# Performance work log

Measured on AMD Instinct MI355X. Metric: run time of the kernel, lower is better.

The kernel has to match this reference:

```python
import jax, jax.numpy as jnp
import numpy as np

G = 16        # groups / heads
DG = 128      # per-group dim (2048/16)
F = 2048      # feat dim (representation_size)
N = 2048      # num_rois
M = 2048      # num_nongt_rois


def setup_inputs() -> dict:
    key = jax.random.key(0)
    ks = jax.random.split(key, 8)
    std = np.float32(0.02)
    return {
        "roi_feat": jax.random.normal(ks[0], (N, F), jnp.float32),
        "ref_feat": jax.random.normal(ks[1], (M, F), jnp.float32),
        "Wq_w": jax.random.normal(ks[2], (F, F), jnp.float32) * std,
        "Wq_b": jnp.zeros((F,), jnp.float32),
        "Wk_w": jax.random.normal(ks[3], (F, F), jnp.float32) * std,
        "Wk_b": jnp.zeros((F,), jnp.float32),
        # grouped 1x1 conv weight [2048, 2048, 1, 1] squeezed to [F, F];
        # group g maps input channels [g*F_g_in] -> output channels [g*DG:(g+1)*DG]
        "Wv_w": jax.random.normal(ks[4], (F, F), jnp.float32) * np.float32(0.01),
        "Wv_b": jnp.zeros((F,), jnp.float32),
    }


def reference(roi_feat, ref_feat, Wq_w, Wq_b, Wk_w, Wk_b, Wv_w, Wv_b):
    n = roi_feat.shape[0]
    scale = np.float32(1.0 / np.sqrt(DG))
    # torch Linear: y = x @ W.T + b
    q = (roi_feat @ Wq_w.T + Wq_b).reshape(n, G, DG)      # [N, G, DG]
    k = (ref_feat @ Wk_w.T + Wk_b).reshape(-1, G, DG)     # [M, G, DG]
    aff = jnp.einsum("ngd,mgd->ngm", q, k) * scale        # [N, G, M]
    attn = jax.nn.softmax(aff, axis=-1)
    # weighted values: v is raw ref_feat, per original
    ov = jnp.einsum("ngm,mf->ngf", attn, ref_feat)        # [N, G, F]
    # grouped 1x1 conv: per-group linear F -> DG
    Wv3 = Wv_w.reshape(G, DG, F)                          # [G, DG, F]
    out = jnp.einsum("ngf,gdf->ngd", ov, Wv3) + Wv_b.reshape(G, DG)
    return out.reshape(n, G * DG)                          # [N, F]
```

## Files before the change

### kernel.cpp

```cpp
#include <hip/hip_runtime.h>
#include <hip/hip_bf16.h>

#define G_   16
#define DG_  128
#define F_   2048
#define N_   2048
#define M_   2048

typedef __attribute__((ext_vector_type(8))) short s16x8;
typedef __attribute__((ext_vector_type(4))) float f32x4;
typedef __attribute__((ext_vector_type(2))) unsigned int u32x2;

typedef const __attribute__((address_space(1))) void GV;
typedef __attribute__((address_space(3))) void LV;

__device__ inline unsigned short f2bf(float f) {
  unsigned u = __float_as_uint(f);
  u += 0x7fffu + ((u >> 16) & 1u);
  return (unsigned short)(u >> 16);
}

struct Cvt5Args { const float* s[5]; unsigned short* d[5]; };

__global__ __launch_bounds__(256)
void cvt5(Cvt5Args a) {
  unsigned u = blockIdx.x * 256 + threadIdx.x;
  if (u >= 5u * 524288u) return;
  int seg = u >> 19;
  unsigned off = u & 524287u;
  const float4* sp = (const float4*)(a.s[seg] + (size_t)off * 8);
  float4 x = sp[0], y = sp[1];
  uint4 o;
  o.x = (unsigned)f2bf(x.x) | ((unsigned)f2bf(x.y) << 16);
  o.y = (unsigned)f2bf(x.z) | ((unsigned)f2bf(x.w) << 16);
  o.z = (unsigned)f2bf(y.x) | ((unsigned)f2bf(y.y) << 16);
  o.w = (unsigned)f2bf(y.z) | ((unsigned)f2bf(y.w) << 16);
  *(uint4*)(a.d[seg] + (size_t)off * 8) = o;
}

struct GemmJobs {
  const unsigned short* A[3];
  const unsigned short* B[3];
  const float* bias[3];
  unsigned short* C[3];
  float osc[3];
};

__global__ __launch_bounds__(512, 2)
void gemm8(GemmJobs jb) {
  __shared__ __align__(16) char lds[131072];
  const int wg = (blockIdx.x & 7) * 24 + (blockIdx.x >> 3);
  const int j  = wg >> 6;
  const int bs = wg & 63;
  const unsigned short* A = jb.A[j];
  const unsigned short* B = jb.B[j];
  const float* bias = jb.bias[j];
  unsigned short* C = jb.C[j];
  const float osc = jb.osc[j];

  const int tid = threadIdx.x, lane = tid & 63, wv = tid >> 6;
  const int wm = wv >> 2, wn = wv & 3;
  const int l15 = lane & 15, l4 = lane >> 4;
  const int m0 = (bs >> 3) * 256, n0 = (bs & 7) * 256;
  const int slot = (l4 ^ ((l15 >> 1) & 3)) * 16;
  const int scol = (((lane & 3) ^ ((lane >> 3) & 3)) * 8);
  const int srow = wv * 16 + (lane >> 2);
  const int rA = wm * 128 + l15;
  const int rB = (wn >> 1) * 128 + (wn & 1) * 64 + l15;

  f32x4 acc[8][4];
#pragma unroll
  for (int i = 0; i < 8; ++i)
#pragma unroll
    for (int nf = 0; nf < 4; ++nf) acc[i][nf] = (f32x4){0.f, 0.f, 0.f, 0.f};

  auto stage_kh = [&](int buf2, int h, int k0) {
#pragma unroll
    for (int rb = 0; rb < 2; ++rb) {
      __builtin_amdgcn_global_load_lds(
          (GV*)(A + (size_t)(m0 + rb * 128 + srow) * F_ + k0 + h * 32 + scol),
          (LV*)(lds + buf2 * 65536 + h * 16384 + rb * 8192 + wv * 1024),
          16, 0, 0);
      __builtin_amdgcn_global_load_lds(
          (GV*)(B + (size_t)(n0 + rb * 128 + srow) * F_ + k0 + h * 32 + scol),
          (LV*)(lds + buf2 * 65536 + 32768 + h * 16384 + rb * 8192 + wv * 1024),
          16, 0, 0);
    }
  };

  stage_kh(0, 0, 0);
  stage_kh(0, 1, 0);
  asm volatile("s_waitcnt vmcnt(4)" ::: "memory");
  __builtin_amdgcn_sched_barrier(0);
  __builtin_amdgcn_s_barrier();

  const int NT = F_ / 64;
  for (int t = 0; t < NT; ++t) {
    const int buf = t & 1;
    const char* Lb = lds + buf * 65536;
    const bool pf = (t + 1 < NT);
    const int k1 = (t + 1) * 64;
    s16x8 af[8], bf[4];

    auto ldA = [&](int mf, int h) {
      return *(const s16x8*)(Lb + h * 16384 + (rA + mf * 16) * 64 + slot);
    };
    auto ldB = [&](int nf, int h) {
      return *(const s16x8*)(Lb + 32768 + h * 16384 + (rB + nf * 16) * 64 + slot);
    };

#pragma unroll
    for (int nf = 0; nf < 4; ++nf) bf[nf] = ldB(nf, 0);
#pragma unroll
    for (int i = 0; i < 8; ++i) af[i] = ldA(i, 0);
    if (pf) stage_kh(buf ^ 1, 0, k1);
    __builtin_amdgcn_sched_barrier(0);
    __builtin_amdgcn_s_barrier();
    asm volatile("s_waitcnt lgkmcnt(0)" ::: "memory");
    __builtin_amdgcn_sched_barrier(0);
    __builtin_amdgcn_s_setprio(1);
#pragma unroll
    for (int i = 0; i < 8; ++i)
#pragma unroll
      for (int nf = 0; nf < 4; ++nf)
        acc[i][nf] = __builtin_amdgcn_mfma_f32_16x16x32_bf16(af[i], bf[nf], acc[i][nf], 0, 0, 0);
    __builtin_amdgcn_s_setprio(0);
    __builtin_amdgcn_sched_barrier(0);

    if (pf) { asm volatile("s_waitcnt vmcnt(4)" ::: "memory"); }
    else    { asm volatile("s_waitcnt vmcnt(0)" ::: "memory"); }
    __builtin_amdgcn_sched_barrier(0);
    __builtin_amdgcn_s_barrier();
#pragma unroll
    for (int nf = 0; nf < 4; ++nf) bf[nf] = ldB(nf, 1);
#pragma unroll
    for (int i = 0; i < 8; ++i) af[i] = ldA(i, 1);
    if (pf) stage_kh(buf ^ 1, 1, k1);
    __builtin_amdgcn_sched_barrier(0);
    __builtin_amdgcn_s_barrier();
    asm volatile("s_waitcnt lgkmcnt(0)" ::: "memory");
    __builtin_amdgcn_sched_barrier(0);
    __builtin_amdgcn_s_setprio(1);
#pragma unroll
    for (int i = 0; i < 8; ++i)
#pragma unroll
      for (int nf = 0; nf < 4; ++nf)
        acc[i][nf] = __builtin_amdgcn_mfma_f32_16x16x32_bf16(af[i], bf[nf], acc[i][nf], 0, 0, 0);
    __builtin_amdgcn_s_setprio(0);
    __builtin_amdgcn_sched_barrier(0);

    if (pf) { asm volatile("s_waitcnt vmcnt(4)" ::: "memory"); }
    __builtin_amdgcn_sched_barrier(0);
    __builtin_amdgcn_s_barrier();
  }

#pragma unroll
  for (int nf = 0; nf < 4; ++nf) {
    int c = n0 + wn * 64 + nf * 16 + l15;
    float bv = bias ? bias[c] : 0.f;
#pragma unroll
    for (int mf = 0; mf < 8; ++mf) {
#pragma unroll
      for (int jj = 0; jj < 4; ++jj) {
        int r = m0 + wm * 128 + mf * 16 + l4 * 4 + jj;
        C[(size_t)r * F_ + c] = f2bf((acc[mf][nf][jj] + bv) * osc);
      }
    }
  }
}

__global__ __launch_bounds__(256, 2)
void attn_mfma(const unsigned short* __restrict__ Q,
               const unsigned short* __restrict__ K,
               const unsigned short* __restrict__ Vt,
               const float* __restrict__ vb,
               float* __restrict__ out) {
  __shared__ unsigned short Kt[2][64 * 128];
  __shared__ unsigned short Vts[2][128 * 64];
  __shared__ unsigned short Pt[4][16 * 64];
  const int tid = threadIdx.x, lane = tid & 63, wv = tid >> 6;
  const int l15 = lane & 15, l4 = lane >> 4;
  const int g = blockIdx.y;
  const int q0 = blockIdx.x * 64 + wv * 16;

  s16x8 qa[4];
#pragma unroll
  for (int kc = 0; kc < 4; ++kc)
    qa[kc] = *(const s16x8*)(Q + (size_t)(q0 + l15) * F_ + g * DG_ + kc * 32 + l4 * 8);

  f32x4 oa[8];
#pragma unroll
  for (int df = 0; df < 8; ++df) oa[df] = (f32x4){0.f, 0.f, 0.f, 0.f};
  float m_r = -1e30f, l_r = 0.f;

  const int ksw0 = (((lane & 15) ^ (lane >> 4)) * 8);
  const int ksw1 = (((lane & 15) ^ 4 ^ (lane >> 4)) * 8);
  const int vsw  = (((lane & 7) ^ (lane >> 3)) * 8);
  const int xorb = (l15 & 7) << 4;
  int csw[4];
#pragma unroll
  for (int kc = 0; kc < 4; ++kc) csw[kc] = (kc * 64 + l4 * 16) ^ xorb;

  auto stage = [&](int buf, int kv0) {
#pragma unroll
    for (int i = 0; i < 4; ++i) {
      int r0 = wv * 16 + i * 4;
      __builtin_amdgcn_global_load_lds(
          (GV*)(K + (size_t)(kv0 + r0 + (lane >> 4)) * F_ + g * DG_ + ((i & 1) ? ksw1 : ksw0)),
          (LV*)(&Kt[buf][r0 * 128]), 16, 0, 0);
    }
#pragma unroll
    for (int i = 0; i < 4; ++i) {
      int r0 = wv * 32 + i * 8;
      __builtin_amdgcn_global_load_lds(
          (GV*)(Vt + (size_t)(g * DG_ + r0 + (lane >> 3)) * M_ + kv0 + vsw),
          (LV*)(&Vts[buf][r0 * 64]), 16, 0, 0);
    }
  };

  stage(0, 0);
  __syncthreads();
  int cur = 0;
  unsigned short* Pw = &Pt[wv][0];

  for (int t = 0; t < M_ / 64; ++t) {
    if (t + 1 < M_ / 64) stage(cur ^ 1, (t + 1) * 64);
    const unsigned short* Kb = &Kt[cur][0];
    const unsigned short* Vb = &Vts[cur][0];

    f32x4 sf[4];
    __builtin_amdgcn_s_setprio(1);
#pragma unroll
    for (int kvf = 0; kvf < 4; ++kvf) {
      f32x4 s = (f32x4){0.f, 0.f, 0.f, 0.f};
#pragma unroll
      for (int kc = 0; kc < 4; ++kc) {
        s16x8 kf = *(const s16x8*)((const char*)Kb + (kvf * 16 + l15) * 256 + csw[kc]);
        s = __builtin_amdgcn_mfma_f32_16x16x32_bf16(kf, qa[kc], s, 0, 0, 0);
      }
      sf[kvf] = s;
    }
    __builtin_amdgcn_s_setprio(0);

    float tmax = sf[0][0];
#pragma unroll
    for (int kvf = 0; kvf < 4; ++kvf) {
      tmax = fmaxf(tmax, fmaxf(fmaxf(sf[kvf][0], sf[kvf][1]),
                               fmaxf(sf[kvf][2], sf[kvf][3])));
    }
    tmax = fmaxf(tmax, __shfl_xor(tmax, 16));
    tmax = fmaxf(tmax, __shfl_xor(tmax, 32));
    if (!__all(tmax <= m_r + 8.0f)) {
      float mnew = fmaxf(m_r, tmax);
      float corr = __builtin_amdgcn_exp2f(m_r - mnew);
      m_r = mnew;
      l_r *= corr;
      float c0 = __shfl(corr, l4 * 4 + 0);
      float c1 = __shfl(corr, l4 * 4 + 1);
      float c2 = __shfl(corr, l4 * 4 + 2);
      float c3 = __shfl(corr, l4 * 4 + 3);
#pragma unroll
      for (int df = 0; df < 8; ++df) {
        oa[df][0] *= c0; oa[df][1] *= c1; oa[df][2] *= c2; oa[df][3] *= c3;
      }
    }

    float psum = 0.f;
#pragma unroll
    for (int kvf = 0; kvf < 4; ++kvf) {
      float p0 = __builtin_amdgcn_exp2f(sf[kvf][0] - m_r);
      float p1 = __builtin_amdgcn_exp2f(sf[kvf][1] - m_r);
      float p2 = __builtin_amdgcn_exp2f(sf[kvf][2] - m_r);
      float p3 = __builtin_amdgcn_exp2f(sf[kvf][3] - m_r);
      psum += (p0 + p1) + (p2 + p3);
      u32x2 w;
      asm("v_cvt_pk_bf16_f32 %0, %1, %2" : "=v"(w.x) : "v"(p0), "v"(p1));
      asm("v_cvt_pk_bf16_f32 %0, %1, %2" : "=v"(w.y) : "v"(p2), "v"(p3));
      *(u32x2*)((char*)Pw + l15 * 128 + ((kvf * 32 + l4 * 8) ^ xorb)) = w;
    }
    psum += __shfl_xor(psum, 16);
    psum += __shfl_xor(psum, 32);
    l_r += psum;

    s16x8 pa0 = *(const s16x8*)((const char*)Pw + l15 * 128 + csw[0]);
    s16x8 pa1 = *(const s16x8*)((const char*)Pw + l15 * 128 + csw[1]);
    __builtin_amdgcn_s_setprio(1);
#pragma unroll
    for (int df = 0; df < 8; ++df) {
      s16x8 v0 = *(const s16x8*)((const char*)Vb + (df * 16 + l15) * 128 + csw[0]);
      s16x8 v1 = *(const s16x8*)((const char*)Vb + (df * 16 + l15) * 128 + csw[1]);
      oa[df] = __builtin_amdgcn_mfma_f32_16x16x32_bf16(pa0, v0, oa[df], 0, 0, 0);
      oa[df] = __builtin_amdgcn_mfma_f32_16x16x32_bf16(pa1, v1, oa[df], 0, 0, 0);
    }
    __builtin_amdgcn_s_setprio(0);
    __syncthreads();
    cur ^= 1;
  }

  float linv = 1.0f / l_r;
  float i0 = __shfl(linv, l4 * 4 + 0);
  float i1 = __shfl(linv, l4 * 4 + 1);
  float i2 = __shfl(linv, l4 * 4 + 2);
  float i3 = __shfl(linv, l4 * 4 + 3);
#pragma unroll
  for (int df = 0; df < 8; ++df) {
    int c = g * DG_ + df * 16 + l15;
    float bv = vb[c];
    out[(size_t)(q0 + l4 * 4 + 0) * F_ + c] = oa[df][0] * i0 + bv;
    out[(size_t)(q0 + l4 * 4 + 1) * F_ + c] = oa[df][1] * i1 + bv;
    out[(size_t)(q0 + l4 * 4 + 2) * F_ + c] = oa[df][2] * i2 + bv;
    out[(size_t)(q0 + l4 * 4 + 3) * F_ + c] = oa[df][3] * i3 + bv;
  }
}

extern "C" void kernel_launch(void* const* d_in, const int* in_sizes, int n_in,
                              void* d_out, int out_size, void* d_ws, size_t ws_size,
                              hipStream_t stream) {
  const float* roi  = (const float*)d_in[0];
  const float* ref  = (const float*)d_in[1];
  const float* Wq_w = (const float*)d_in[2];
  const float* Wq_b = (const float*)d_in[3];
  const float* Wk_w = (const float*)d_in[4];
  const float* Wk_b = (const float*)d_in[5];
  const float* Wv_w = (const float*)d_in[6];
  const float* Wv_b = (const float*)d_in[7];
  float* out = (float*)d_out;
  const size_t SEG = 4194304;
  const float cscale = 0.12751664508246770f;

  if (ws_size < 64ull * 1024 * 1024) return;
  unsigned short* roi_bf = (unsigned short*)d_ws;
  unsigned short* ref_bf = roi_bf + SEG;
  unsigned short* Wq_bf  = ref_bf + SEG;
  unsigned short* Wk_bf  = Wq_bf + SEG;
  unsigned short* Wv_bf  = Wk_bf + SEG;
  unsigned short* Qb     = Wv_bf + SEG;
  unsigned short* Kb     = Qb + SEG;
  unsigned short* Vtb    = Kb + SEG;

  Cvt5Args ca;
  ca.s[0] = roi;  ca.d[0] = roi_bf;
  ca.s[1] = ref;  ca.d[1] = ref_bf;
  ca.s[2] = Wq_w; ca.d[2] = Wq_bf;
  ca.s[3] = Wk_w; ca.d[3] = Wk_bf;
  ca.s[4] = Wv_w; ca.d[4] = Wv_bf;
  cvt5<<<10240, 256, 0, stream>>>(ca);

  GemmJobs jb;
  jb.A[0] = roi_bf; jb.B[0] = Wq_bf;  jb.bias[0] = Wq_b;    jb.C[0] = Qb;  jb.osc[0] = cscale;
  jb.A[1] = ref_bf; jb.B[1] = Wk_bf;  jb.bias[1] = Wk_b;    jb.C[1] = Kb;  jb.osc[1] = 1.0f;
  jb.A[2] = Wv_bf;  jb.B[2] = ref_bf; jb.bias[2] = nullptr; jb.C[2] = Vtb; jb.osc[2] = 1.0f;
  gemm8<<<192, 512, 0, stream>>>(jb);

  attn_mfma<<<dim3(N_ / 64, G_), 256, 0, stream>>>(Qb, Kb, Vtb, Wv_b, out);
}
```

Before: 143.1 us.

## Process two 16-row query fragments per wave to reuse K/V LDS reads

Each wave now handles 32 query rows (two 16-row MFMA fragments) instead of 16, so every K and V fragment loaded from LDS feeds two MFMAs. The block covers 128 queries and the grid halves to 256 blocks. This cuts LDS read traffic and staging per unit of work, but raises register pressure (double accumulators and score tiles) and halves the block count, which may lower occupancy on a 256-CU device.

New measurement: 149.9 us. 4.7% more time.

```diff
diff --git a/kernel.cpp b/kernel.cpp
--- a/kernel.cpp
+++ b/kernel.cpp
@@ -177,21 +177,25 @@
                float* __restrict__ out) {
   __shared__ unsigned short Kt[2][64 * 128];
   __shared__ unsigned short Vts[2][128 * 64];
-  __shared__ unsigned short Pt[4][16 * 64];
+  __shared__ unsigned short Pt[4][32 * 64];
   const int tid = threadIdx.x, lane = tid & 63, wv = tid >> 6;
   const int l15 = lane & 15, l4 = lane >> 4;
   const int g = blockIdx.y;
-  const int q0 = blockIdx.x * 64 + wv * 16;
-
-  s16x8 qa[4];
-#pragma unroll
-  for (int kc = 0; kc < 4; ++kc)
-    qa[kc] = *(const s16x8*)(Q + (size_t)(q0 + l15) * F_ + g * DG_ + kc * 32 + l4 * 8);
-
-  f32x4 oa[8];
-#pragma unroll
-  for (int df = 0; df < 8; ++df) oa[df] = (f32x4){0.f, 0.f, 0.f, 0.f};
-  float m_r = -1e30f, l_r = 0.f;
+  const int q0 = blockIdx.x * 128 + wv * 32;
+
+  s16x8 qa[2][4];
+#pragma unroll
+  for (int qf = 0; qf < 2; ++qf)
+#pragma unroll
+    for (int kc = 0; kc < 4; ++kc)
+      qa[qf][kc] = *(const s16x8*)(Q + (size_t)(q0 + qf * 16 + l15) * F_ + g * DG_ + kc * 32 + l4 * 8);
+
+  f32x4 oa[8][2];
+#pragma unroll
+  for (int df = 0; df < 8; ++df)
+#pragma unroll
+    for (int qf = 0; qf < 2; ++qf) oa[df][qf] = (f32x4){0.f, 0.f, 0.f, 0.f};
+  float m_r[2] = {-1e30f, -1e30f}, l_r[2] = {0.f, 0.f};
 
   const int ksw0 = (((lane & 15) ^ (lane >> 4)) * 8);
   const int ksw1 = (((lane & 15) ^ 4 ^ (lane >> 4)) * 8);
@@ -228,88 +232,115 @@
     const unsigned short* Kb = &Kt[cur][0];
     const unsigned short* Vb = &Vts[cur][0];
 
-    f32x4 sf[4];
+    f32x4 sf[4][2];
     __builtin_amdgcn_s_setprio(1);
 #pragma unroll
     for (int kvf = 0; kvf < 4; ++kvf) {
-      f32x4 s = (f32x4){0.f, 0.f, 0.f, 0.f};
+      s16x8 kf[4];
+#pragma unroll
+      for (int kc = 0; kc < 4; ++kc)
+        kf[kc] = *(const s16x8*)((const char*)Kb + (kvf * 16 + l15) * 256 + csw[kc]);
+      f32x4 s0 = (f32x4){0.f, 0.f, 0.f, 0.f};
+      f32x4 s1 = (f32x4){0.f, 0.f, 0.f, 0.f};
 #pragma unroll
       for (int kc = 0; kc < 4; ++kc) {
-        s16x8 kf = *(const s16x8*)((const char*)Kb + (kvf * 16 + l15) * 256 + csw[kc]);
-        s = __builtin_amdgcn_mfma_f32_16x16x32_bf16(kf, qa[kc], s, 0, 0, 0);
+        s0 = __builtin_amdgcn_mfma_f32_16x16x32_bf16(kf[kc], qa[0][kc], s0, 0, 0, 0);
+        s1 = __builtin_amdgcn_mfma_f32_16x16x32_bf16(kf[kc], qa[1][kc], s1, 0, 0, 0);
       }
-      sf[kvf] = s;
+      sf[kvf][0] = s0;
+      sf[kvf][1] = s1;
     }
     __builtin_amdgcn_s_setprio(0);
 
-    float tmax = sf[0][0];
-#pragma unroll
-    for (int kvf = 0; kvf < 4; ++kvf) {
-      tmax = fmaxf(tmax, fmaxf(fmaxf(sf[kvf][0], sf[kvf][1]),
-                               fmaxf(sf[kvf][2], sf[kvf][3])));
-    }
-    tmax = fmaxf(tmax, __shfl_xor(tmax, 16));
-    tmax = fmaxf(tmax, __shfl_xor(tmax, 32));
-    if (!__all(tmax <= m_r + 8.0f)) {
-      float mnew = fmaxf(m_r, tmax);
-      float corr = __builtin_amdgcn_exp2f(m_r - mnew);
-      m_r = mnew;
-      l_r *= corr;
-      float c0 = __shfl(corr, l4 * 4 + 0);
-      float c1 = __shfl(corr, l4 * 4 + 1);
-      float c2 = __shfl(corr, l4 * 4 + 2);
-      float c3 = __shfl(corr, l4 * 4 + 3);
-#pragma unroll
-      for (int df = 0; df < 8; ++df) {
-        oa[df][0] *= c0; oa[df][1] *= c1; oa[df][2] *= c2; oa[df][3] *= c3;
+    float tmax[2];
+#pragma unroll
+    for (int qf = 0; qf < 2; ++qf) {
+      float tm = sf[0][qf][0];
+#pragma unroll
+      for (int kvf = 0; kvf < 4; ++kvf)
+        tm = fmaxf(tm, fmaxf(fmaxf(sf[kvf][qf][0], sf[kvf][qf][1]),
+                             fmaxf(sf[kvf][qf][2], sf[kvf][qf][3])));
+      tm = fmaxf(tm, __shfl_xor(tm, 16));
+      tm = fmaxf(tm, __shfl_xor(tm, 32));
+      tmax[qf] = tm;
+    }
+    if (!__all(tmax[0] <= m_r[0] + 8.0f && tmax[1] <= m_r[1] + 8.0f)) {
+#pragma unroll
+      for (int qf = 0; qf < 2; ++qf) {
+        float mnew = fmaxf(m_r[qf], tmax[qf]);
+        float corr = __builtin_amdgcn_exp2f(m_r[qf] - mnew);
+        m_r[qf] = mnew;
+        l_r[qf] *= corr;
+        float c0 = __shfl(corr, l4 * 4 + 0);
+        float c1 = __shfl(corr, l4 * 4 + 1);
+        float c2 = __shfl(corr, l4 * 4 + 2);
+        float c3 = __shfl(corr, l4 * 4 + 3);
+#pragma unroll
+        for (int df = 0; df < 8; ++df) {
+          oa[df][qf][0] *= c0; oa[df][qf][1] *= c1;
+          oa[df][qf][2] *= c2; oa[df][qf][3] *= c3;
+        }
       }
     }
 
-    float psum = 0.f;
-#pragma unroll
-    for (int kvf = 0; kvf < 4; ++kvf) {
-      float p0 = __builtin_amdgcn_exp2f(sf[kvf][0] - m_r);
-      float p1 = __builtin_amdgcn_exp2f(sf[kvf][1] - m_r);
-      float p2 = __builtin_amdgcn_exp2f(sf[kvf][2] - m_r);
-      float p3 = __builtin_amdgcn_exp2f(sf[kvf][3] - m_r);
-      psum += (p0 + p1) + (p2 + p3);
-      u32x2 w;
-      asm("v_cvt_pk_bf16_f32 %0, %1, %2" : "=v"(w.x) : "v"(p0), "v"(p1));
-      asm("v_cvt_pk_bf16_f32 %0, %1, %2" : "=v"(w.y) : "v"(p2), "v"(p3));
-      *(u32x2*)((char*)Pw + l15 * 128 + ((kvf * 32 + l4 * 8) ^ xorb)) = w;
-    }
-    psum += __shfl_xor(psum, 16);
-    psum += __shfl_xor(psum, 32);
-    l_r += psum;
-
-    s16x8 pa0 = *(const s16x8*)((const char*)Pw + l15 * 128 + csw[0]);
-    s16x8 pa1 = *(const s16x8*)((const char*)Pw + l15 * 128 + csw[1]);
+#pragma unroll
+    for (int qf = 0; qf < 2; ++qf) {
+      float psum = 0.f;
+#pragma unroll
+      for (int kvf = 0; kvf < 4; ++kvf) {
+        float p0 = __builtin_amdgcn_exp2f(sf[kvf][qf][0] - m_r[qf]);
+        float p1 = __builtin_amdgcn_exp2f(sf[kvf][qf][1] - m_r[qf]);
+        float p2 = __builtin_amdgcn_exp2f(sf[kvf][qf][2] - m_r[qf]);
+        float p3 = __builtin_amdgcn_exp2f(sf[kvf][qf][3] - m_r[qf]);
+        psum += (p0 + p1) + (p2 + p3);
+        u32x2 w;
+        asm("v_cvt_pk_bf16_f32 %0, %1, %2" : "=v"(w.x) : "v"(p0), "v"(p1));
+        asm("v_cvt_pk_bf16_f32 %0, %1, %2" : "=v"(w.y) : "v"(p2), "v"(p3));
+        *(u32x2*)((char*)Pw + (qf * 16 + l15) * 128 + ((kvf * 32 + l4 * 8) ^ xorb)) = w;
+      }
+      psum += __shfl_xor(psum, 16);
+      psum += __shfl_xor(psum, 32);
+      l_r[qf] += psum;
+    }
+
+    s16x8 pa[2][2];
+#pragma unroll
+    for (int qf = 0; qf < 2; ++qf)
+#pragma unroll
+      for (int kc2 = 0; kc2 < 2; ++kc2)
+        pa[qf][kc2] = *(const s16x8*)((const char*)Pw + (qf * 16 + l15) * 128 + csw[kc2]);
     __builtin_amdgcn_s_setprio(1);
 #pragma unroll
     for (int df = 0; df < 8; ++df) {
       s16x8 v0 = *(const s16x8*)((const char*)Vb + (df * 16 + l15) * 128 + csw[0]);
       s16x8 v1 = *(const s16x8*)((const char*)Vb + (df * 16 + l15) * 128 + csw[1]);
-      oa[df] = __builtin_amdgcn_mfma_f32_16x16x32_bf16(pa0, v0, oa[df], 0, 0, 0);
-      oa[df] = __builtin_amdgcn_mfma_f32_16x16x32_bf16(pa1, v1, oa[df], 0, 0, 0);
+      oa[df][0] = __builtin_amdgcn_mfma_f32_16x16x32_bf16(pa[0][0], v0, oa[df][0], 0, 0, 0);
+      oa[df][0] = __builtin_amdgcn_mfma_f32_16x16x32_bf16(pa[0][1], v1, oa[df][0], 0, 0, 0);
+      oa[df][1] = __builtin_amdgcn_mfma_f32_16x16x32_bf16(pa[1][0], v0, oa[df][1], 0, 0, 0);
+      oa[df][1] = __builtin_amdgcn_mfma_f32_16x16x32_bf16(pa[1][1], v1, oa[df][1], 0, 0, 0);
     }
     __builtin_amdgcn_s_setprio(0);
     __syncthreads();
     cur ^= 1;
   }
 
-  float linv = 1.0f / l_r;
-  float i0 = __shfl(linv, l4 * 4 + 0);
-  float i1 = __shfl(linv, l4 * 4 + 1);
-  float i2 = __shfl(linv, l4 * 4 + 2);
-  float i3 = __shfl(linv, l4 * 4 + 3);
-#pragma unroll
-  for (int df = 0; df < 8; ++df) {
-    int c = g * DG_ + df * 16 + l15;
-    float bv = vb[c];
-    out[(size_t)(q0 + l4 * 4 + 0) * F_ + c] = oa[df][0] * i0 + bv;
-    out[(size_t)(q0 + l4 * 4 + 1) * F_ + c] = oa[df][1] * i1 + bv;
-    out[(size_t)(q0 + l4 * 4 + 2) * F_ + c] = oa[df][2] * i2 + bv;
-    out[(size_t)(q0 + l4 * 4 + 3) * F_ + c] = oa[df][3] * i3 + bv;
+#pragma unroll
+  for (int qf = 0; qf < 2; ++qf) {
+    float linv = 1.0f / l_r[qf];
+    float i0 = __shfl(linv, l4 * 4 + 0);
+    float i1 = __shfl(linv, l4 * 4 + 1);
+    float i2 = __shfl(linv, l4 * 4 + 2);
+    float i3 = __shfl(linv, l4 * 4 + 3);
+#pragma unroll
+    for (int df = 0; df < 8; ++df) {
+      int c = g * DG_ + df * 16 + l15;
+      float bv = vb[c];
+      int r = q0 + qf * 16 + l4 * 4;
+      out[(size_t)(r + 0) * F_ + c] = oa[df][qf][0] * i0 + bv;
+      out[(size_t)(r + 1) * F_ + c] = oa[df][qf][1] * i1 + bv;
+      out[(size_t)(r + 2) * F_ + c] = oa[df][qf][2] * i2 + bv;
+      out[(size_t)(r + 3) * F_ + c] = oa[df][qf][3] * i3 + bv;
+    }
   }
 }
 
@@ -352,5 +383,5 @@
   jb.A[2] = Wv_bf;  jb.B[2] = ref_bf; jb.bias[2] = nullptr; jb.C[2] = Vtb; jb.osc[2] = 1.0f;
   gemm8<<<192, 512, 0, stream>>>(jb);
 
-  attn_mfma<<<dim3(N_ / 64, G_), 256, 0, stream>>>(Qb, Kb, Vtb, Wv_b, out);
-}
+  attn_mfma<<<dim3(N_ / 128, G_), 256, 0, stream>>>(Qb, Kb, Vtb, Wv_b, out);
+}
```
